# Kernel optimization log

Hardware: AMD Instinct MI355X
Metric: run time of the kernel (lower is better)

## Reference

```python
import jax, jax.numpy as jnp
import numpy as np

N_NODES = 50000
N_EDGES = 600000
IN_DIM, HID, OUT_DIM, N_LAYERS = 256, 128, 10, 3
BN_EPS = 1e-5


def setup_inputs() -> dict:
    key = jax.random.key(0)
    ks = jax.random.split(key, 12)
    x = jax.random.normal(ks[0], (N_NODES, IN_DIM), dtype=jnp.float32)
    edge_index = jax.random.randint(ks[1], (2, N_EDGES), 0, N_NODES, dtype=jnp.int64)
    s = 0.05
    W_in = jax.random.normal(ks[2], (IN_DIM, HID), dtype=jnp.float32) * s
    b_in = jnp.zeros((HID,), dtype=jnp.float32)
    Wc = jax.random.normal(ks[3], (N_LAYERS, HID, HID), dtype=jnp.float32) * s
    bc = jnp.zeros((N_LAYERS, HID), dtype=jnp.float32)
    gamma = jnp.ones((N_LAYERS, HID), dtype=jnp.float32)
    beta = jnp.zeros((N_LAYERS, HID), dtype=jnp.float32)
    W_out = jax.random.normal(ks[4], (HID, OUT_DIM), dtype=jnp.float32) * s
    b_out = jnp.zeros((OUT_DIM,), dtype=jnp.float32)
    return {"x": x, "edge_index": edge_index, "W_in": W_in, "b_in": b_in,
            "Wc": Wc, "bc": bc, "gamma": gamma, "beta": beta,
            "W_out": W_out, "b_out": b_out}


def gcn_conv(h, src, dst, W, b):
    # PyG GCNConv: add self-loops, D^{-1/2} A_hat D^{-1/2} (h W) + b
    h = h @ W  # [N, HID]
    deg = jax.ops.segment_sum(jnp.ones((src.shape[0],), h.dtype), dst,
                              num_segments=N_NODES) + 1.0  # self-loop
    dinv = jax.lax.rsqrt(deg)  # deg >= 1
    norm = dinv[src] * dinv[dst]  # [E]
    msg = h[src] * norm[:, None]  # gather + scale
    agg = jax.ops.segment_sum(msg, dst, num_segments=N_NODES)
    agg = agg + h * (dinv * dinv)[:, None]  # self-loop term
    return agg + b


def batchnorm(h, g, be):
    mu = jnp.mean(h, axis=0)
    var = jnp.mean((h - mu) ** 2, axis=0)  # biased, as torch BN
    return (h - mu) * jax.lax.rsqrt(var + BN_EPS) * g + be


def reference(x, edge_index, W_in, b_in, Wc, bc, gamma, beta, W_out, b_out):
    src, dst = edge_index[0], edge_index[1]
    h = jax.nn.relu(x @ W_in + b_in)
    for i in range(N_LAYERS):
        h_res = h
        h = gcn_conv(h, src, dst, Wc[i], bc[i])
        h = batchnorm(h, gamma[i], beta[i])
        h = jax.nn.relu(h)  # dropout = identity (eval mode)
        if i > 0:
            h = h + h_res
    return h @ W_out + b_out
```

## Files before the change

kernel.cpp:

```cpp
#include <hip/hip_runtime.h>

#define N_NODES 50000
#define N_EDGES 600000
#define IN_DIM 256
#define HID 128
#define OUT_DIM 10
#define BN_EPS 1e-5f
#define CAP 64

typedef unsigned int uint32;
typedef unsigned short ushort_t;
typedef __attribute__((ext_vector_type(8))) short short8;
typedef __attribute__((ext_vector_type(4))) float float4v;

__device__ __forceinline__ unsigned short f2bf_rne(float f) {
    uint32 u = __float_as_uint(f);
    u += 0x7FFF + ((u >> 16) & 1);
    return (unsigned short)(u >> 16);
}
__device__ __forceinline__ float bf_lo(uint32 v) { return __uint_as_float(v << 16); }
__device__ __forceinline__ float bf_hi(uint32 v) { return __uint_as_float(v & 0xFFFF0000u); }
__device__ __forceinline__ float bfs(unsigned short s) { return __uint_as_float((uint32)s << 16); }

#define ZERO_UINT4 18656
#define ZERO_BLK 73

__global__ __launch_bounds__(256) void zero_pack_kernel(uint4* __restrict__ zbase,
                                                        const float* __restrict__ W_in,
                                                        const float* __restrict__ Wc,
                                                        unsigned short* __restrict__ PWin,
                                                        unsigned short* __restrict__ PWc) {
    if (blockIdx.x < ZERO_BLK) {
        int i = blockIdx.x * 256 + threadIdx.x;
        if (i < ZERO_UINT4) {
            uint4 z; z.x = 0; z.y = 0; z.z = 0; z.w = 0;
            zbase[i] = z;
        }
        return;
    }
    int idx = (blockIdx.x - ZERO_BLK) * 256 + threadIdx.x;
    if (idx >= 4096 + 3 * 2048) return;
    const float* W;
    unsigned short* P;
    int r;
    if (idx < 4096) { W = W_in; P = PWin + (size_t)idx * 8; r = idx; }
    else {
        int t = idx - 4096;
        int layer = t / 2048;
        r = t - layer * 2048;
        W = Wc + (size_t)layer * HID * HID;
        P = PWc + (size_t)(layer * 2048 + r) * 8;
    }
    int lane = r & 63;
    int nt = (r >> 6) & 7;
    int kt = r >> 9;
    int n = nt * 16 + (lane & 15);
    int kbase = kt * 32 + (lane >> 4) * 8;
    #pragma unroll
    for (int j = 0; j < 8; ++j) P[j] = f2bf_rne(W[(size_t)(kbase + j) * HID + n]);
}


#define FILL_BLK 586

__global__ __launch_bounds__(256) void fill_gemm_in(const int* __restrict__ src,
                                                    const int* __restrict__ dst,
                                                    float* __restrict__ cntf,
                                                    ushort_t* __restrict__ col,
                                                    const float* __restrict__ x,
                                                    const unsigned short* __restrict__ PWin,
                                                    const unsigned short* __restrict__ PWc0,
                                                    const float* __restrict__ b_in,
                                                    unsigned short* __restrict__ B16, int M) {
    __shared__ unsigned short As[64 * 264];
    unsigned short* Hs = As;
    int tid = threadIdx.x;

    int bid = blockIdx.x;
    int gid;
    if ((bid & 1) == 0) {
        gid = bid >> 1;
    } else {
        int f = bid >> 1;
        if (f < FILL_BLK) {
            int e0 = (f * 256 + tid) * 4;
            if (e0 < N_EDGES) {
                int4 d4 = *(const int4*)(dst + e0);
                int4 s4 = *(const int4*)(src + e0);
                int p0 = (int)atomicAdd(&cntf[d4.x], 1.0f);
                int p1 = (int)atomicAdd(&cntf[d4.y], 1.0f);
                int p2 = (int)atomicAdd(&cntf[d4.z], 1.0f);
                int p3 = (int)atomicAdd(&cntf[d4.w], 1.0f);
                if (p0 < CAP) col[(size_t)d4.x * CAP + p0] = (ushort_t)s4.x;
                if (p1 < CAP) col[(size_t)d4.y * CAP + p1] = (ushort_t)s4.y;
                if (p2 < CAP) col[(size_t)d4.z * CAP + p2] = (ushort_t)s4.z;
                if (p3 < CAP) col[(size_t)d4.w * CAP + p3] = (ushort_t)s4.w;
            }
            return;
        }
        gid = f + 98;
    }

    int w = tid >> 6, lane = tid & 63;
    int mrow = lane & 15, quad = lane >> 4;
    int m0 = gid * 64;

    int r = tid >> 2;
    int cq = tid & 3;
    int row = m0 + r;

    if (row < M) {
        const float* xr = x + (size_t)row * IN_DIM;
        #pragma unroll
        for (int c = 0; c < 8; ++c) {
            const float* srcp = xr + c * 32 + cq * 8;
            float4 a0 = *(const float4*)(srcp);
            float4 a1 = *(const float4*)(srcp + 4);
            short8 pk;
            pk[0] = (short)f2bf_rne(a0.x); pk[1] = (short)f2bf_rne(a0.y);
            pk[2] = (short)f2bf_rne(a0.z); pk[3] = (short)f2bf_rne(a0.w);
            pk[4] = (short)f2bf_rne(a1.x); pk[5] = (short)f2bf_rne(a1.y);
            pk[6] = (short)f2bf_rne(a1.z); pk[7] = (short)f2bf_rne(a1.w);
            *(short8*)&As[r * 264 + c * 32 + cq * 8] = pk;
        }
    } else {
        short8 z;
        #pragma unroll
        for (int j = 0; j < 8; ++j) z[j] = 0;
        #pragma unroll
        for (int c = 0; c < 8; ++c) *(short8*)&As[r * 264 + c * 32 + cq * 8] = z;
    }
    __syncthreads();

    float4v acc[8];
    #pragma unroll
    for (int nt = 0; nt < 8; ++nt)
        #pragma unroll
        for (int i = 0; i < 4; ++i) acc[nt][i] = 0.f;

    #pragma unroll
    for (int kt = 0; kt < 8; ++kt) {
        short8 afrag = *(const short8*)&As[(w * 16 + mrow) * 264 + kt * 32 + quad * 8];
        const unsigned short* pb = PWin + ((size_t)(kt * 8) * 64 + lane) * 8;
        #pragma unroll
        for (int nt = 0; nt < 8; ++nt) {
            short8 bfrag = *(const short8*)(pb + (size_t)nt * 64 * 8);
            acc[nt] = __builtin_amdgcn_mfma_f32_16x16x32_bf16(afrag, bfrag, acc[nt], 0, 0, 0);
        }
    }
    __syncthreads();

    int rl = w * 16 + quad * 4;
    #pragma unroll
    for (int nt = 0; nt < 8; ++nt) {
        int col_ = nt * 16 + mrow;
        float bv = b_in[col_];
        #pragma unroll
        for (int reg = 0; reg < 4; ++reg) {
            float h = fmaxf(acc[nt][reg] + bv, 0.f);
            Hs[(rl + reg) * 136 + col_] = f2bf_rne(h);
        }
    }
    __syncthreads();

    float4v acc2[8];
    #pragma unroll
    for (int nt = 0; nt < 8; ++nt)
        #pragma unroll
        for (int i = 0; i < 4; ++i) acc2[nt][i] = 0.f;

    #pragma unroll
    for (int kt = 0; kt < 4; ++kt) {
        short8 af2 = *(const short8*)&Hs[(w * 16 + mrow) * 136 + kt * 32 + quad * 8];
        const unsigned short* pb = PWc0 + ((size_t)(kt * 8) * 64 + lane) * 8;
        #pragma unroll
        for (int nt = 0; nt < 8; ++nt) {
            short8 bfrag = *(const short8*)(pb + (size_t)nt * 64 * 8);
            acc2[nt] = __builtin_amdgcn_mfma_f32_16x16x32_bf16(af2, bfrag, acc2[nt], 0, 0, 0);
        }
    }

    int rowbase = m0 + w * 16 + quad * 4;
    #pragma unroll
    for (int nt = 0; nt < 8; ++nt) {
        int col_ = nt * 16 + mrow;
        #pragma unroll
        for (int reg = 0; reg < 4; ++reg) {
            int rw = rowbase + reg;
            if (rw < M) B16[(size_t)rw * HID + col_] = f2bf_rne(acc2[nt][reg]);
        }
    }
}


template <int PRE>
__global__ __launch_bounds__(256) void agg_stats_kernel(const uint32* __restrict__ Bs32,
                                                        const float* __restrict__ cntf,
                                                        const ushort_t* __restrict__ col,
                                                        const float* __restrict__ bc,
                                                        uint32* __restrict__ C16,
                                                        float* __restrict__ colsum_multi) {
    __shared__ float shs[4][128];
    __shared__ float shq[4][128];
    int lane = threadIdx.x;
    int ty = threadIdx.y;
    int n = blockIdx.x * 4 + ty;
    int h = lane >> 5;
    int c = lane & 31;
    int sh = h << 4;

    const uint2* B2 = (const uint2*)Bs32;
    float cn = cntf[n];
    int deg = (int)cn;
    if (deg > CAP) deg = CAP;
    float dn = rsqrtf(cn + 1.0f);

    float a0 = 0.f, a1 = 0.f, a2 = 0.f, a3 = 0.f;
    if (h == 0) {
        uint2 vs = B2[(size_t)n * 32 + c];
        if (PRE) {
            a0 = bf_lo(vs.x); a1 = bf_hi(vs.x);
            a2 = bf_lo(vs.y); a3 = bf_hi(vs.y);
        } else {
            a0 = dn * bf_lo(vs.x); a1 = dn * bf_hi(vs.x);
            a2 = dn * bf_lo(vs.y); a3 = dn * bf_hi(vs.y);
        }
    }

    const uint4* cb = (const uint4*)(col + (size_t)n * CAP);
    int e = 0;
    for (; e + 16 <= deg; e += 16) {
        uint4 q0 = cb[e >> 3];
        uint4 q1 = cb[(e >> 3) + 1];
        int s[8];
        s[0] = (q0.x >> sh) & 0xFFFF; s[1] = (q0.y >> sh) & 0xFFFF;
        s[2] = (q0.z >> sh) & 0xFFFF; s[3] = (q0.w >> sh) & 0xFFFF;
        s[4] = (q1.x >> sh) & 0xFFFF; s[5] = (q1.y >> sh) & 0xFFFF;
        s[6] = (q1.z >> sh) & 0xFFFF; s[7] = (q1.w >> sh) & 0xFFFF;
        float cg[8];
        if (!PRE) {
            #pragma unroll
            for (int k = 0; k < 8; ++k) cg[k] = cntf[s[k]];
        }
        uint2 v[8];
        #pragma unroll
        for (int k = 0; k < 8; ++k) v[k] = B2[(size_t)s[k] * 32 + c];
        #pragma unroll
        for (int k = 0; k < 8; ++k) {
            if (PRE) {
                a0 += bf_lo(v[k].x); a1 += bf_hi(v[k].x);
                a2 += bf_lo(v[k].y); a3 += bf_hi(v[k].y);
            } else {
                float wk = rsqrtf(cg[k] + 1.0f);
                a0 += wk * bf_lo(v[k].x); a1 += wk * bf_hi(v[k].x);
                a2 += wk * bf_lo(v[k].y); a3 += wk * bf_hi(v[k].y);
            }
        }
    }
    if (e < deg) {
        uint4 q0 = cb[e >> 3];
        uint4 q1 = cb[(e >> 3) + 1];
        int rem = deg - e;
        int sfirst = (int)(q0.x & 0xFFFFu);
        uint32 dw[8] = {q0.x, q0.y, q0.z, q0.w, q1.x, q1.y, q1.z, q1.w};
        int s[8]; float msk[8];
        #pragma unroll
        for (int k = 0; k < 8; ++k) {
            int valid = (2 * k + h) < rem;
            s[k] = valid ? (int)((dw[k] >> sh) & 0xFFFFu) : sfirst;
            msk[k] = valid ? 1.f : 0.f;
        }
        float cg[8];
        if (!PRE) {
            #pragma unroll
            for (int k = 0; k < 8; ++k) cg[k] = cntf[s[k]];
        }
        uint2 v[8];
        #pragma unroll
        for (int k = 0; k < 8; ++k) v[k] = B2[(size_t)s[k] * 32 + c];
        #pragma unroll
        for (int k = 0; k < 8; ++k) {
            float wk = PRE ? msk[k] : (msk[k] * rsqrtf(cg[k] + 1.0f));
            a0 += wk * bf_lo(v[k].x); a1 += wk * bf_hi(v[k].x);
            a2 += wk * bf_lo(v[k].y); a3 += wk * bf_hi(v[k].y);
        }
    }

    a0 += __shfl_xor(a0, 32, 64);
    a1 += __shfl_xor(a1, 32, 64);
    a2 += __shfl_xor(a2, 32, 64);
    a3 += __shfl_xor(a3, 32, 64);

    float4 bcv = *(const float4*)(bc + c * 4);
    float o0 = a0 * dn + bcv.x;
    float o1 = a1 * dn + bcv.y;
    float o2 = a2 * dn + bcv.z;
    float o3 = a3 * dn + bcv.w;

    float e0 = h ? o2 : o0;
    float e1 = h ? o3 : o1;
    C16[(size_t)n * 64 + c * 2 + h] = (uint32)f2bf_rne(e0) | ((uint32)f2bf_rne(e1) << 16);

    int f = c * 4 + h * 2;
    shs[ty][f] = e0;       shs[ty][f + 1] = e1;
    shq[ty][f] = e0 * e0;  shq[ty][f + 1] = e1 * e1;
    __syncthreads();
    int t = ty * 64 + lane;
    if (t < 128) {
        float s = shs[0][t] + shs[1][t] + shs[2][t] + shs[3][t];
        float q = shq[0][t] + shq[1][t] + shq[2][t] + shq[3][t];
        float* base = colsum_multi + (size_t)(blockIdx.x & 31) * 256;
        atomicAdd(&base[t], s);
        atomicAdd(&base[t + 128], q);
    }
}


template <int RES>
__global__ __launch_bounds__(256) void gemm_bn_fused(const unsigned short* __restrict__ C16,
                                                     const unsigned short* __restrict__ PB,
                                                     const float* __restrict__ colsum_multi,
                                                     const float* __restrict__ gamma,
                                                     const float* __restrict__ beta,
                                                     const float* __restrict__ cntf,
                                                     unsigned short* __restrict__ A16,
                                                     unsigned short* __restrict__ B16, int M) {
    __shared__ unsigned short As[64 * 136];
    __shared__ float scs[128], shb[128];
    int tid = threadIdx.x;
    int w = tid >> 6, lane = tid & 63;
    int mrow = lane & 15, quad = lane >> 4;
    int m0 = blockIdx.x * 64;

    if (tid < 128) {
        float s = 0.f, q = 0.f;
        #pragma unroll
        for (int cc = 0; cc < 32; ++cc) {
            s += colsum_multi[cc * 256 + tid];
            q += colsum_multi[cc * 256 + tid + 128];
        }
        float mu = s * (1.0f / N_NODES);
        float var = q * (1.0f / N_NODES) - mu * mu;
        float rstd = rsqrtf(var + BN_EPS);
        float sc = rstd * gamma[tid];
        scs[tid] = sc;
        shb[tid] = beta[tid] - mu * sc;
    }

    int r = tid >> 2;
    int cq = tid & 3;
    int row = m0 + r;
    bool vrow = row < M;
    short8 cv[4], av[4];
    if (vrow) {
        #pragma unroll
        for (int u = 0; u < 4; ++u)
            cv[u] = *(const short8*)(C16 + (size_t)row * HID + cq * 32 + u * 8);
        if (RES) {
            #pragma unroll
            for (int u = 0; u < 4; ++u)
                av[u] = *(const short8*)(A16 + (size_t)row * HID + cq * 32 + u * 8);
        }
    }
    __syncthreads();

    if (vrow) {
        #pragma unroll
        for (int u = 0; u < 4; ++u) {
            int col0 = cq * 32 + u * 8;
            short8 pk;
            #pragma unroll
            for (int j = 0; j < 8; ++j) {
                float h = fmaxf(bfs((unsigned short)cv[u][j]) * scs[col0 + j] + shb[col0 + j], 0.f);
                if (RES) h += bfs((unsigned short)av[u][j]);
                pk[j] = (short)f2bf_rne(h);
            }
            *(short8*)(A16 + (size_t)row * HID + col0) = pk;
            *(short8*)&As[r * 136 + col0] = pk;
        }
    } else {
        short8 z;
        #pragma unroll
        for (int j = 0; j < 8; ++j) z[j] = 0;
        #pragma unroll
        for (int u = 0; u < 4; ++u) *(short8*)&As[r * 136 + cq * 32 + u * 8] = z;
    }
    __syncthreads();

    float4v acc[8];
    #pragma unroll
    for (int nt = 0; nt < 8; ++nt)
        #pragma unroll
        for (int i = 0; i < 4; ++i) acc[nt][i] = 0.f;

    #pragma unroll
    for (int kt = 0; kt < 4; ++kt) {
        short8 afrag = *(const short8*)&As[(w * 16 + mrow) * 136 + kt * 32 + quad * 8];
        const unsigned short* pb = PB + ((size_t)(kt * 8) * 64 + lane) * 8;
        #pragma unroll
        for (int nt = 0; nt < 8; ++nt) {
            short8 bfrag = *(const short8*)(pb + (size_t)nt * 64 * 8);
            acc[nt] = __builtin_amdgcn_mfma_f32_16x16x32_bf16(afrag, bfrag, acc[nt], 0, 0, 0);
        }
    }

    int rowbase = m0 + w * 16 + quad * 4;
    float rs[4];
    #pragma unroll
    for (int reg = 0; reg < 4; ++reg) {
        int rw = rowbase + reg;
        rs[reg] = (rw < M) ? rsqrtf(cntf[rw] + 1.0f) : 0.f;
    }
    #pragma unroll
    for (int nt = 0; nt < 8; ++nt) {
        int col = nt * 16 + mrow;
        #pragma unroll
        for (int reg = 0; reg < 4; ++reg) {
            int rw = rowbase + reg;
            if (rw < M) B16[(size_t)rw * HID + col] = f2bf_rne(acc[nt][reg] * rs[reg]);
        }
    }
}


__global__ void out_fused(const uint32* __restrict__ C16,
                          const uint32* __restrict__ A16,
                          const float* __restrict__ colsum_multi,
                          const float* __restrict__ gamma,
                          const float* __restrict__ beta,
                          const float* __restrict__ Wo,
                          const float* __restrict__ bo,
                          float* __restrict__ out) {
    __shared__ float Hs[64][132];
    __shared__ float WoS[HID * OUT_DIM];
    __shared__ float scs[128], shb[128];
    int tid = threadIdx.x;
    for (int i = tid; i < HID * OUT_DIM; i += 256) WoS[i] = Wo[i];
    if (tid < 128) {
        float s = 0.f, q = 0.f;
        #pragma unroll
        for (int cc = 0; cc < 32; ++cc) {
            s += colsum_multi[cc * 256 + tid];
            q += colsum_multi[cc * 256 + tid + 128];
        }
        float mu = s * (1.0f / N_NODES);
        float var = q * (1.0f / N_NODES) - mu * mu;
        float rstd = rsqrtf(var + BN_EPS);
        float sc = rstd * gamma[tid];
        scs[tid] = sc;
        shb[tid] = beta[tid] - mu * sc;
    }
    __syncthreads();

    int n0 = blockIdx.x * 64;
    #pragma unroll
    for (int i = 0; i < 8; ++i) {
        int lin = i * 256 + tid;
        int row = lin >> 5;
        int colq = lin & 31;
        int n = n0 + row;
        float4 h = make_float4(0.f, 0.f, 0.f, 0.f);
        if (n < N_NODES) {
            uint2 cv = ((const uint2*)C16)[(size_t)n * 32 + colq];
            uint2 av = ((const uint2*)A16)[(size_t)n * 32 + colq];
            float c0 = bf_lo(cv.x), c1 = bf_hi(cv.x), c2 = bf_lo(cv.y), c3 = bf_hi(cv.y);
            float4 s = *(const float4*)(scs + colq * 4);
            float4 t = *(const float4*)(shb + colq * 4);
            h.x = fmaxf(c0 * s.x + t.x, 0.f) + bf_lo(av.x);
            h.y = fmaxf(c1 * s.y + t.y, 0.f) + bf_hi(av.x);
            h.z = fmaxf(c2 * s.z + t.z, 0.f) + bf_lo(av.y);
            h.w = fmaxf(c3 * s.w + t.w, 0.f) + bf_hi(av.y);
        }
        *(float4*)&Hs[row][colq * 4] = h;
    }
    __syncthreads();

    #pragma unroll
    for (int j = 0; j < 3; ++j) {
        int o = j * 256 + tid;
        if (o < 64 * OUT_DIM) {
            int nl = o / OUT_DIM;
            int c = o - nl * OUT_DIM;
            int n = n0 + nl;
            if (n < N_NODES) {
                float s = 0.f;
                #pragma unroll 4
                for (int k = 0; k < HID; ++k) s += Hs[nl][k] * WoS[k * OUT_DIM + c];
                out[(size_t)n * OUT_DIM + c] = s + bo[c];
            }
        }
    }
}


extern "C" void kernel_launch(void* const* d_in, const int* in_sizes, int n_in,
                              void* d_out, int out_size, void* d_ws, size_t ws_size,
                              hipStream_t stream) {
    const float* x     = (const float*)d_in[0];
    const int*   ei    = (const int*)d_in[1];
    const int*   src   = ei;
    const int*   dst   = ei + N_EDGES;
    const float* W_in  = (const float*)d_in[2];
    const float* b_in  = (const float*)d_in[3];
    const float* Wc    = (const float*)d_in[4];
    const float* bc    = (const float*)d_in[5];
    const float* gamma = (const float*)d_in[6];
    const float* beta  = (const float*)d_in[7];
    const float* W_out = (const float*)d_in[8];
    const float* b_out = (const float*)d_in[9];
    float* out = (float*)d_out;

    char* p = (char*)d_ws;
    auto alloc = [&](size_t bytes) -> char* {
        char* q = p;
        p += (bytes + 255) & ~(size_t)255;
        return q;
    };
    float* cntf      = (float*)alloc(sizeof(float) * N_NODES);
    float* colsumAll = (float*)alloc(sizeof(float) * 3 * 32 * 256);
    unsigned short* A16 = (unsigned short*)alloc(sizeof(unsigned short) * N_NODES * HID);
    unsigned short* B16 = (unsigned short*)alloc(sizeof(unsigned short) * N_NODES * HID);
    uint32* C16       = (uint32*)alloc(sizeof(unsigned short) * N_NODES * HID);
    ushort_t* col     = (ushort_t*)alloc(sizeof(ushort_t) * N_NODES * CAP);
    unsigned short* PWin = (unsigned short*)alloc(sizeof(unsigned short) * 4096 * 8);
    unsigned short* PWc  = (unsigned short*)alloc(sizeof(unsigned short) * 3 * 2048 * 8);

    const int gblk = (N_NODES + 63) / 64;

    zero_pack_kernel<<<ZERO_BLK + 40, 256, 0, stream>>>((uint4*)cntf, W_in, Wc, PWin, PWc);

    fill_gemm_in<<<FILL_BLK + gblk, 256, 0, stream>>>(src, dst, cntf, col,
                                                      x, PWin, PWc, b_in, B16, N_NODES);

    for (int l = 0; l < 3; ++l) {
        float* colsum = colsumAll + (size_t)l * 32 * 256;
        if (l == 0) {
            agg_stats_kernel<0><<<N_NODES / 4, dim3(64, 4), 0, stream>>>(
                (const uint32*)B16, cntf, col, bc + l * HID, C16, colsum);
        } else {
            agg_stats_kernel<1><<<N_NODES / 4, dim3(64, 4), 0, stream>>>(
                (const uint32*)B16, cntf, col, bc + l * HID, C16, colsum);
        }
        if (l == 0) {
            gemm_bn_fused<0><<<gblk, 256, 0, stream>>>(
                (const unsigned short*)C16, PWc + (size_t)1 * 2048 * 8, colsum,
                gamma, beta, cntf, A16, B16, N_NODES);
        } else if (l == 1) {
            gemm_bn_fused<1><<<gblk, 256, 0, stream>>>(
                (const unsigned short*)C16, PWc + (size_t)2 * 2048 * 8, colsum,
                gamma + HID, beta + HID, cntf, A16, B16, N_NODES);
        } else {
            out_fused<<<gblk, 256, 0, stream>>>(
                C16, (const uint32*)A16, colsum, gamma + 2 * HID, beta + 2 * HID, W_out, b_out, out);
        }
    }
}
```

Before: 276.8 us.

## Pre-convert x to bf16 in prep kernel; transpose W_out in LDS for vector dot

The fp32-to-bf16 conversion of the input features moves out of the fused fill/GEMM kernel into a separate pass in the prep kernel, which writes a bf16 copy of x to workspace. The input GEMM then reads half the bytes. Overall traffic goes up, though: x is read once in fp32 and written and read again in bf16, so this only pays off if the GEMM load was the bottleneck overlapping with the fill work. Separately, the output projection stores W_out transposed in shared memory and uses float4 LDS reads for the dot product.

```diff
diff --git a/kernel.cpp b/kernel.cpp
--- a/kernel.cpp
+++ b/kernel.cpp
@@ -22,23 +22,40 @@
 __device__ __forceinline__ float bf_hi(uint32 v) { return __uint_as_float(v & 0xFFFF0000u); }
 __device__ __forceinline__ float bfs(unsigned short s) { return __uint_as_float((uint32)s << 16); }
 
+#define XCVT_BLK 6250
 #define ZERO_UINT4 18656
 #define ZERO_BLK 73
 
-__global__ __launch_bounds__(256) void zero_pack_kernel(uint4* __restrict__ zbase,
-                                                        const float* __restrict__ W_in,
-                                                        const float* __restrict__ Wc,
-                                                        unsigned short* __restrict__ PWin,
-                                                        unsigned short* __restrict__ PWc) {
-    if (blockIdx.x < ZERO_BLK) {
-        int i = blockIdx.x * 256 + threadIdx.x;
+__global__ __launch_bounds__(256) void prep_kernel(const float* __restrict__ x,
+                                                   unsigned short* __restrict__ x16,
+                                                   uint4* __restrict__ zbase,
+                                                   const float* __restrict__ W_in,
+                                                   const float* __restrict__ Wc,
+                                                   unsigned short* __restrict__ PWin,
+                                                   unsigned short* __restrict__ PWc) {
+    int bid = blockIdx.x;
+    if (bid < XCVT_BLK) {
+        int t = bid * 256 + threadIdx.x;
+        const float* srcp = x + (size_t)t * 8;
+        float4 a0 = *(const float4*)(srcp);
+        float4 a1 = *(const float4*)(srcp + 4);
+        short8 pk;
+        pk[0] = (short)f2bf_rne(a0.x); pk[1] = (short)f2bf_rne(a0.y);
+        pk[2] = (short)f2bf_rne(a0.z); pk[3] = (short)f2bf_rne(a0.w);
+        pk[4] = (short)f2bf_rne(a1.x); pk[5] = (short)f2bf_rne(a1.y);
+        pk[6] = (short)f2bf_rne(a1.z); pk[7] = (short)f2bf_rne(a1.w);
+        *(short8*)(x16 + (size_t)t * 8) = pk;
+        return;
+    }
+    if (bid < XCVT_BLK + ZERO_BLK) {
+        int i = (bid - XCVT_BLK) * 256 + threadIdx.x;
         if (i < ZERO_UINT4) {
             uint4 z; z.x = 0; z.y = 0; z.z = 0; z.w = 0;
             zbase[i] = z;
         }
         return;
     }
-    int idx = (blockIdx.x - ZERO_BLK) * 256 + threadIdx.x;
+    int idx = (bid - XCVT_BLK - ZERO_BLK) * 256 + threadIdx.x;
     if (idx >= 4096 + 3 * 2048) return;
     const float* W;
     unsigned short* P;
@@ -67,7 +84,7 @@
                                                     const int* __restrict__ dst,
                                                     float* __restrict__ cntf,
                                                     ushort_t* __restrict__ col,
-                                                    const float* __restrict__ x,
+                                                    const unsigned short* __restrict__ x16,
                                                     const unsigned short* __restrict__ PWin,
                                                     const unsigned short* __restrict__ PWc0,
                                                     const float* __restrict__ b_in,
@@ -110,17 +127,10 @@
     int row = m0 + r;
 
     if (row < M) {
-        const float* xr = x + (size_t)row * IN_DIM;
+        const unsigned short* xr = x16 + (size_t)row * IN_DIM;
         #pragma unroll
         for (int c = 0; c < 8; ++c) {
-            const float* srcp = xr + c * 32 + cq * 8;
-            float4 a0 = *(const float4*)(srcp);
-            float4 a1 = *(const float4*)(srcp + 4);
-            short8 pk;
-            pk[0] = (short)f2bf_rne(a0.x); pk[1] = (short)f2bf_rne(a0.y);
-            pk[2] = (short)f2bf_rne(a0.z); pk[3] = (short)f2bf_rne(a0.w);
-            pk[4] = (short)f2bf_rne(a1.x); pk[5] = (short)f2bf_rne(a1.y);
-            pk[6] = (short)f2bf_rne(a1.z); pk[7] = (short)f2bf_rne(a1.w);
+            short8 pk = *(const short8*)(xr + c * 32 + cq * 8);
             *(short8*)&As[r * 264 + c * 32 + cq * 8] = pk;
         }
     } else {
@@ -432,10 +442,14 @@
                           const float* __restrict__ bo,
                           float* __restrict__ out) {
     __shared__ float Hs[64][132];
-    __shared__ float WoS[HID * OUT_DIM];
+    __shared__ float WoT[OUT_DIM][132];
     __shared__ float scs[128], shb[128];
     int tid = threadIdx.x;
-    for (int i = tid; i < HID * OUT_DIM; i += 256) WoS[i] = Wo[i];
+    for (int i = tid; i < HID * OUT_DIM; i += 256) {
+        int k = i / OUT_DIM;
+        int c = i - k * OUT_DIM;
+        WoT[c][k] = Wo[i];
+    }
     if (tid < 128) {
         float s = 0.f, q = 0.f;
         #pragma unroll
@@ -484,8 +498,15 @@
             int n = n0 + nl;
             if (n < N_NODES) {
                 float s = 0.f;
-                #pragma unroll 4
-                for (int k = 0; k < HID; ++k) s += Hs[nl][k] * WoS[k * OUT_DIM + c];
+                #pragma unroll 8
+                for (int k = 0; k < HID; k += 4) {
+                    float4 hv = *(const float4*)&Hs[nl][k];
+                    float4 wv = *(const float4*)&WoT[c][k];
+                    s += hv.x * wv.x;
+                    s += hv.y * wv.y;
+                    s += hv.z * wv.z;
+                    s += hv.w * wv.w;
+                }
                 out[(size_t)n * OUT_DIM + c] = s + bo[c];
             }
         }
@@ -524,13 +545,15 @@
     ushort_t* col     = (ushort_t*)alloc(sizeof(ushort_t) * N_NODES * CAP);
     unsigned short* PWin = (unsigned short*)alloc(sizeof(unsigned short) * 4096 * 8);
     unsigned short* PWc  = (unsigned short*)alloc(sizeof(unsigned short) * 3 * 2048 * 8);
+    unsigned short* x16  = (unsigned short*)alloc(sizeof(unsigned short) * N_NODES * IN_DIM);
 
     const int gblk = (N_NODES + 63) / 64;
 
-    zero_pack_kernel<<<ZERO_BLK + 40, 256, 0, stream>>>((uint4*)cntf, W_in, Wc, PWin, PWc);
+    prep_kernel<<<XCVT_BLK + ZERO_BLK + 40, 256, 0, stream>>>(
+        x, x16, (uint4*)cntf, W_in, Wc, PWin, PWc);
 
     fill_gemm_in<<<FILL_BLK + gblk, 256, 0, stream>>>(src, dst, cntf, col,
-                                                      x, PWin, PWc, b_in, B16, N_NODES);
+                                                      x16, PWin, PWc, b_in, B16, N_NODES);
 
     for (int l = 0; l < 3; ++l) {
         float* colsum = colsumAll + (size_t)l * 32 * 256;
```

After: 286.5 us. 1.03x slower.
